# Performance work log

Measured on AMD Instinct MI355X. Metric: run time of the kernel, lower is better.

Reference implementation:

```python
import jax, jax.numpy as jnp
import numpy as np

BS, S, DM, H, DK, DV, PRED = 64, 128, 512, 8, 512, 512, 96
NF = S * DM  # Flatten_Head nf = patch_num * d_model
SCALE_INIT = (DM // H) ** (-0.5)  # head_dim from d_model//n_heads per _ScaledDotProductAttention


def setup_inputs() -> dict:
    key = jax.random.key(0)
    ks = jax.random.split(key, 24)
    g = lambda k, shp: (0.02 * jax.random.normal(k, shp)).astype(jnp.float32)
    inp = {
        "x": jax.random.normal(ks[0], (BS, S, DM), dtype=jnp.float32),
        "prev": jax.random.normal(ks[1], (BS, H, S, S), dtype=jnp.float32),
        # multi-head attention projections (d_k = d_v = d_model per TMBlock)
        "Wq": g(ks[2], (DM, H * DK)), "bq": jnp.zeros((H * DK,), jnp.float32),
        "Wk": g(ks[3], (DM, H * DK)), "bk": jnp.zeros((H * DK,), jnp.float32),
        "Wv": g(ks[4], (DM, H * DV)), "bv": jnp.zeros((H * DV,), jnp.float32),
        "Wo": g(ks[5], (H * DV, DM)), "bo": jnp.zeros((DM,), jnp.float32),
        "scale": jnp.float32(SCALE_INIT),
        # InterPatchMixing: Linear(PatchNum, PatchNum) x2
        "Wi1": g(ks[6], (S, S)), "bi1": jnp.zeros((S,), jnp.float32),
        "Wi2": g(ks[7], (S, S)), "bi2": jnp.zeros((S,), jnp.float32),
        # IntraPatchMixing: Linear(PatchEmbedDim, PatchEmbedDim) x2
        "Wt1": g(ks[8], (DM, DM)), "bt1": jnp.zeros((DM,), jnp.float32),
        "Wt2": g(ks[9], (DM, DM)), "bt2": jnp.zeros((DM,), jnp.float32),
        # Flatten_Head (non-individual): Linear(nf, pred_len)
        "Wh": g(ks[10], (NF, PRED)), "bh": jnp.zeros((PRED,), jnp.float32),
    }
    return inp


def reference(x, prev, Wq, bq, Wk, bk, Wv, bv, Wo, bo, scale,
              Wi1, bi1, Wi2, bi2, Wt1, bt1, Wt2, bt2, Wh, bh):
    bs = x.shape[0]
    # projections -> [bs, H, S, d]
    q = (x @ Wq + bq).reshape(bs, S, H, DK).transpose(0, 2, 1, 3)
    k = (x @ Wk + bk).reshape(bs, S, H, DK).transpose(0, 2, 1, 3)
    v = (x @ Wv + bv).reshape(bs, S, H, DV).transpose(0, 2, 1, 3)
    # manual scaled dot-product attention with residual attention bias (Realformer)
    scores = jnp.einsum('bhqd,bhkd->bhqk', q, k) * scale + prev
    attn = jax.nn.softmax(scores, axis=-1)  # dropout is identity at eval
    o = jnp.einsum('bhqk,bhkd->bhqd', attn, v)
    o = o.transpose(0, 2, 1, 3).reshape(bs, S, H * DV)
    o = o @ Wo + bo  # [bs, S, DM]
    # InterPatchMixing over the patch axis (last dim must be PatchNum)
    t = o.transpose(0, 2, 1)  # [bs, DM, S]
    t = jax.nn.relu(t @ Wi1 + bi1) @ Wi2 + bi2
    y = t.transpose(0, 2, 1)  # [bs, S, DM]
    # IntraPatchMixing over embed dim
    z = jax.nn.relu(y @ Wt1 + bt1) @ Wt2 + bt2
    # Flatten_Head: flatten last two dims -> Linear(nf, pred_len)
    out = z.reshape(bs, NF) @ Wh + bh  # [bs, PRED]
    return out
```

## Files before the change

### kernel.cpp

```cpp
#include <hip/hip_runtime.h>
#include <cstdint>
#include <cstddef>

typedef __bf16 bf16_t;
typedef __bf16 bf16x8 __attribute__((ext_vector_type(8)));
typedef __bf16 bf16x4 __attribute__((ext_vector_type(4)));
typedef float  f32x4  __attribute__((ext_vector_type(4)));

#define MFMA(a, b, c) __builtin_amdgcn_mfma_f32_16x16x32_bf16((a), (b), (c), 0, 0, 0)


__global__ __launch_bounds__(256) void k_convert_dual(const float* __restrict__ in,
                                                      bf16_t* __restrict__ xb,
                                                      bf16_t* __restrict__ xT) {
  __shared__ bf16_t tile[32][34];
  int tx = threadIdx.x & 31, ty = threadIdx.x >> 5;
  int c0 = blockIdx.x * 32, r0 = blockIdx.y * 32;
#pragma unroll
  for (int j = 0; j < 4; ++j) {
    int r = r0 + ty + j * 8;
    bf16_t bv = (bf16_t)in[(size_t)r * 512 + c0 + tx];
    xb[(size_t)r * 512 + c0 + tx] = bv;
    tile[ty + j * 8][tx] = bv;
  }
  __syncthreads();
  int b = (r0 + tx) >> 7, s = (r0 + tx) & 127;
#pragma unroll
  for (int j = 0; j < 4; ++j) {
    int i = c0 + ty + j * 8;
    xT[(size_t)b * 65536 + (size_t)i * 128 + s] = tile[tx][ty + j * 8];
  }
}

__global__ __launch_bounds__(256) void k_transpose_convert(const float* __restrict__ in,
                                                           bf16_t* __restrict__ out,
                                                           int R, int C) {
  __shared__ float tile[32][33];
  int tx = threadIdx.x & 31, ty = threadIdx.x >> 5;
  int c0 = blockIdx.x * 32, r0 = blockIdx.y * 32;
#pragma unroll
  for (int j = 0; j < 4; ++j)
    tile[ty + j * 8][tx] = in[(size_t)(r0 + ty + j * 8) * C + c0 + tx];
  __syncthreads();
#pragma unroll
  for (int j = 0; j < 4; ++j)
    out[(size_t)(c0 + ty + j * 8) * R + r0 + tx] = (bf16_t)tile[tx][ty + j * 8];
}

__global__ __launch_bounds__(256) void k_transpose_b16(const bf16_t* __restrict__ in,
                                                       bf16_t* __restrict__ out,
                                                       int R, int C) {
  __shared__ bf16_t tile[32][34];
  size_t base = (size_t)blockIdx.z * R * C;
  int tx = threadIdx.x & 31, ty = threadIdx.x >> 5;
  int c0 = blockIdx.x * 32, r0 = blockIdx.y * 32;
#pragma unroll
  for (int j = 0; j < 4; ++j)
    tile[ty + j * 8][tx] = in[base + (size_t)(r0 + ty + j * 8) * C + c0 + tx];
  __syncthreads();
#pragma unroll
  for (int j = 0; j < 4; ++j)
    out[base + (size_t)(c0 + ty + j * 8) * R + r0 + tx] = tile[tx][ty + j * 8];
}

template <int BMODE>
__global__ __launch_bounds__(256) void k_wprod(const float* __restrict__ Ap,
                                               const float* __restrict__ Bp,
                                               bf16_t* __restrict__ out,
                                               int ldA, int ldB) {
  __shared__ __align__(16) bf16_t As[128 * 68];
  __shared__ __align__(16) bf16_t Bs[128 * 68];
  const int tid = threadIdx.x, lane = tid & 63, wave = tid >> 6;
  const int wr = (wave >> 1) * 64, wc = (wave & 1) * 64;
  const int lr = lane & 15, lk = (lane >> 4) * 8, frow = (lane >> 4) * 4;
  const int m0 = blockIdx.x * 128, n0 = blockIdx.y * 128, h = blockIdx.z;
  const int sr = tid >> 3, sc = (tid & 7) * 8;
  f32x4 acc[4][4] = {};

  for (int kt = 0; kt < 512; kt += 64) {
#pragma unroll
    for (int rr = 0; rr < 4; ++rr) {
      int r = sr + 32 * rr;
      const float* ap = Ap + (size_t)(m0 + r) * ldA + h * 512 + kt + sc;
      bf16x8 av;
#pragma unroll
      for (int e = 0; e < 8; ++e) av[e] = (bf16_t)ap[e];
      *(bf16x8*)(As + r * 68 + sc) = av;
    }
    if (BMODE == 0) {
#pragma unroll
      for (int rr = 0; rr < 4; ++rr) {
        int r = sr + 32 * rr;
        const float* bp = Bp + (size_t)(n0 + r) * ldB + h * 512 + kt + sc;
        bf16x8 bv;
#pragma unroll
        for (int e = 0; e < 8; ++e) bv[e] = (bf16_t)bp[e];
        *(bf16x8*)(Bs + r * 68 + sc) = bv;
      }
    } else {
#pragma unroll
      for (int rr = 0; rr < 8; ++rr) {
        int kr = (tid >> 5) + 8 * rr;
        int nc = (tid & 31) * 4;
        const float* bp = Bp + (size_t)(h * 512 + kt + kr) * ldB + n0 + nc;
        float4 v = *(const float4*)bp;
        Bs[(nc + 0) * 68 + kr] = (bf16_t)v.x;
        Bs[(nc + 1) * 68 + kr] = (bf16_t)v.y;
        Bs[(nc + 2) * 68 + kr] = (bf16_t)v.z;
        Bs[(nc + 3) * 68 + kr] = (bf16_t)v.w;
      }
    }
    __syncthreads();
#pragma unroll
    for (int kk = 0; kk < 2; ++kk) {
      bf16x8 af[4], bfr[4];
#pragma unroll
      for (int i = 0; i < 4; ++i)
        af[i] = *(const bf16x8*)(As + (wr + i * 16 + lr) * 68 + kk * 32 + lk);
#pragma unroll
      for (int j = 0; j < 4; ++j)
        bfr[j] = *(const bf16x8*)(Bs + (wc + j * 16 + lr) * 68 + kk * 32 + lk);
#pragma unroll
      for (int i = 0; i < 4; ++i)
#pragma unroll
        for (int j = 0; j < 4; ++j)
          acc[i][j] = MFMA(af[i], bfr[j], acc[i][j]);
    }
    __syncthreads();
  }
#pragma unroll
  for (int i = 0; i < 4; ++i)
#pragma unroll
    for (int j = 0; j < 4; ++j)
#pragma unroll
      for (int q = 0; q < 4; ++q) {
        int gm = m0 + wr + i * 16 + frow + q;
        int gn = n0 + wc + j * 16 + lr;
        if (BMODE == 0)
          out[(size_t)(h * 512 + gn) * 512 + gm] = (bf16_t)acc[i][j][q];
        else
          out[(size_t)gn * 4096 + h * 512 + gm] = (bf16_t)acc[i][j][q];
      }
}

__global__ __launch_bounds__(256) void k_sbias(const float* __restrict__ Wq,
                                               const float* __restrict__ bk,
                                               const float* __restrict__ Wk,
                                               const float* __restrict__ bq,
                                               float* __restrict__ W1,
                                               float* __restrict__ W2,
                                               float* __restrict__ c) {
  const int lane = threadIdx.x & 63, wave = threadIdx.x >> 6;
  const int i = blockIdx.x * 4 + wave;
  for (int h = 0; h < 8; ++h) {
    float s1 = 0.f, s2 = 0.f;
    for (int d = lane; d < 512; d += 64) {
      s1 += Wq[(size_t)i * 4096 + h * 512 + d] * bk[h * 512 + d];
      s2 += Wk[(size_t)i * 4096 + h * 512 + d] * bq[h * 512 + d];
    }
#pragma unroll
    for (int o = 32; o > 0; o >>= 1) { s1 += __shfl_down(s1, o); s2 += __shfl_down(s2, o); }
    if (lane == 0) { W1[h * 512 + i] = s1; W2[h * 512 + i] = s2; }
  }
  if (blockIdx.x == 0 && wave == 0) {
    for (int h = 0; h < 8; ++h) {
      float cc = 0.f;
      for (int d = lane; d < 512; d += 64) cc += bq[h * 512 + d] * bk[h * 512 + d];
#pragma unroll
      for (int o = 32; o > 0; o >>= 1) cc += __shfl_down(cc, o);
      if (lane == 0) c[h] = cc;
    }
  }
}

__global__ __launch_bounds__(256) void k_tbias(const bf16_t* __restrict__ xb,
                                               const float* __restrict__ W1,
                                               const float* __restrict__ W2,
                                               const float* __restrict__ cb,
                                               float* __restrict__ TallT) {
  __shared__ float Ws[16][512];
  __shared__ float scr[128][32];
  const int tid = threadIdx.x;
  for (int i = tid; i < 4096; i += 256) {
    Ws[i >> 9][i & 511] = W1[i];
    Ws[8 + (i >> 9)][i & 511] = W2[i];
  }
  __syncthreads();
  const int rl = tid & 127, part = tid >> 7;
  const int row = blockIdx.x * 128 + rl;
  const bf16_t* xr = xb + (size_t)row * 512 + part * 256;
  float acc[16] = {};
  for (int i = 0; i < 256; i += 8) {
    bf16x8 xv = *(const bf16x8*)(xr + i);
#pragma unroll
    for (int e = 0; e < 8; ++e) {
      float f = (float)xv[e];
#pragma unroll
      for (int cI = 0; cI < 16; ++cI) acc[cI] += f * Ws[cI][part * 256 + i + e];
    }
  }
#pragma unroll
  for (int cI = 0; cI < 16; ++cI) scr[rl][part * 16 + cI] = acc[cI];
  __syncthreads();
  if (tid < 128) {
    int r = blockIdx.x * 128 + tid;
#pragma unroll
    for (int cI = 0; cI < 16; ++cI) {
      float v = scr[tid][cI] + scr[tid][16 + cI];
      if (cI < 8) v += cb[cI];
      TallT[cI * 8192 + r] = v;
    }
  }
}

__global__ __launch_bounds__(256) void k_cvec1(const float* __restrict__ bv,
                                               const float* __restrict__ Wo,
                                               float* __restrict__ cpart) {
  int cch = blockIdx.x, d = threadIdx.x * 2;
  float ax = 0.f, ay = 0.f;
  for (int n = cch * 128; n < cch * 128 + 128; ++n) {
    float b = bv[n];
    float2 w = *(const float2*)(Wo + (size_t)n * 512 + d);
    ax += b * w.x; ay += b * w.y;
  }
  cpart[(size_t)cch * 512 + d] = ax;
  cpart[(size_t)cch * 512 + d + 1] = ay;
}
__global__ __launch_bounds__(256) void k_cvec2(const float* __restrict__ cpart,
                                               const float* __restrict__ bo,
                                               float* __restrict__ cvec) {
  int d = blockIdx.x * 256 + threadIdx.x;
  float s = bo[d];
  for (int cch = 0; cch < 32; ++cch) s += cpart[(size_t)cch * 512 + d];
  cvec[d] = s;
}

__global__ __launch_bounds__(64, 2) void k_attn7(const bf16_t* __restrict__ xb,
                                                 const bf16_t* __restrict__ xT,
                                                 bf16_t* __restrict__ TU,
                                                 const float* __restrict__ prev,
                                                 const float* __restrict__ scale_p,
                                                 const float* __restrict__ TallT,
                                                 int hg) {
  __shared__ __align__(16) bf16_t Pl[16 * 136];
  __shared__ __align__(16) bf16_t Bw[16 * 72];

  const int lane = threadIdx.x;
  const int lr = lane & 15, lk = (lane >> 4) * 8, frow = (lane >> 4) * 4;
  const int bid = blockIdx.x;
  const int bx = (bid & 7) * 256 + (bid >> 3);
  const int b = bx >> 5, hp = (bx >> 3) & 3, rg = bx & 7;
  const int h = hg * 4 + hp;
  const int r0 = rg * 16;
  const bf16_t* xB = xb + (size_t)b * 65536;
  const bf16_t* xTB = xT + (size_t)b * 65536;
  bf16_t* tB = TU + ((size_t)hp * 8192 + b * 128 + r0) * 512;

  bf16_t tf_store[16 * 8];
  bf16x8* tf = (bf16x8*)tf_store;
  const bf16_t* aP = tB + (size_t)lr * 512 + lk;
#pragma unroll
  for (int kx = 0; kx < 16; ++kx) tf[kx] = *(const bf16x8*)(aP + kx * 32);

  const float* t1p = TallT + h * 8192 + b * 128 + r0;
  const float* t2p = TallT + (8 + h) * 8192 + b * 128;
  float pv[4][8];
#pragma unroll
  for (int e = 0; e < 4; ++e) {
    const float* prow = prev + (((size_t)(b * 8 + h)) * 128 + r0 + frow + e) * 128;
#pragma unroll
    for (int j = 0; j < 8; ++j) pv[e][j] = prow[j * 16 + lr];
  }
  float t1r[4];
#pragma unroll
  for (int e = 0; e < 4; ++e) t1r[e] = t1p[frow + e];
  float t2r[8];
#pragma unroll
  for (int j = 0; j < 8; ++j) t2r[j] = t2p[j * 16 + lr];

  f32x4 sacc[8] = {};
  const bf16_t* bP = xB + (size_t)lr * 512 + lk;
  __builtin_amdgcn_s_setprio(1);
#pragma unroll
  for (int kx = 0; kx < 16; ++kx) {
    bf16x8 bfr[8];
#pragma unroll
    for (int j = 0; j < 8; ++j)
      bfr[j] = *(const bf16x8*)(bP + (size_t)j * 8192 + kx * 32);
#pragma unroll
    for (int j = 0; j < 8; ++j) sacc[j] = MFMA(tf[kx], bfr[j], sacc[j]);
  }
  __builtin_amdgcn_s_setprio(0);

  const float scl = scale_p[0];
#pragma unroll
  for (int e = 0; e < 4; ++e) {
    const int rl = frow + e;
    float mx = -3.4e38f;
#pragma unroll
    for (int j = 0; j < 8; ++j) {
      float v = scl * (sacc[j][e] + t1r[e] + t2r[j]) + pv[e][j];
      sacc[j][e] = v;
      mx = fmaxf(mx, v);
    }
    mx = fmaxf(mx, __shfl_xor(mx, 1));
    mx = fmaxf(mx, __shfl_xor(mx, 2));
    mx = fmaxf(mx, __shfl_xor(mx, 4));
    mx = fmaxf(mx, __shfl_xor(mx, 8));
    float sum = 0.f;
#pragma unroll
    for (int j = 0; j < 8; ++j) {
      float p = __expf(sacc[j][e] - mx);
      sacc[j][e] = p;
      sum += p;
    }
    sum += __shfl_xor(sum, 1);
    sum += __shfl_xor(sum, 2);
    sum += __shfl_xor(sum, 4);
    sum += __shfl_xor(sum, 8);
    float inv = 1.f / sum;
#pragma unroll
    for (int j = 0; j < 8; ++j)
      Pl[rl * 136 + j * 16 + lr] = (bf16_t)(sacc[j][e] * inv);
  }

#pragma unroll
  for (int dc = 0; dc < 8; ++dc) {
    f32x4 oacc[4] = {};
    __builtin_amdgcn_s_setprio(1);
#pragma unroll
    for (int kk = 0; kk < 4; ++kk) {
      bf16x8 pa = *(const bf16x8*)(Pl + lr * 136 + kk * 32 + lk);
      bf16x8 xf[4];
#pragma unroll
      for (int j = 0; j < 4; ++j)
        xf[j] = *(const bf16x8*)(xTB + (size_t)(dc * 64 + j * 16 + lr) * 128 + kk * 32 + lk);
#pragma unroll
      for (int j = 0; j < 4; ++j) oacc[j] = MFMA(pa, xf[j], oacc[j]);
    }
    __builtin_amdgcn_s_setprio(0);
#pragma unroll
    for (int j = 0; j < 4; ++j)
#pragma unroll
      for (int e = 0; e < 4; ++e)
        Bw[(frow + e) * 72 + j * 16 + lr] = (bf16_t)oacc[j][e];
#pragma unroll
    for (int r2 = 0; r2 < 2; ++r2) {
      int row = lane >> 2, chunk = (lane & 3) + r2 * 4;
      *(bf16x8*)(tB + (size_t)row * 512 + dc * 64 + chunk * 8) =
          *(const bf16x8*)(Bw + row * 72 + chunk * 8);
    }
  }
}

template <int OUTMODE, int RELU>
__global__ __launch_bounds__(256) void k_gemm(const bf16_t* __restrict__ A,
                                              const bf16_t* __restrict__ Bt,
                                              const float* __restrict__ bias,
                                              bf16_t* __restrict__ C,
                                              int M, int N, int K) {
  __shared__ __align__(16) bf16_t As[128 * 68];
  __shared__ __align__(16) bf16_t Bs[128 * 68];
  const int tid = threadIdx.x, lane = tid & 63, wave = tid >> 6;
  const int wr = (wave >> 1) * 64, wc = (wave & 1) * 64;
  const int m0 = blockIdx.x * 128, n0 = blockIdx.y * 128;
  const int lr = lane & 15, lk = (lane >> 4) * 8, frow = (lane >> 4) * 4;
  const int sr = tid >> 3, sc = (tid & 7) * 8;
  f32x4 acc[4][4] = {};

  for (int kt = 0; kt < K; kt += 64) {
#pragma unroll
    for (int i = 0; i < 4; ++i) {
      int r = i * 32 + sr;
      *(bf16x8*)(As + r * 68 + sc) = *(const bf16x8*)(A + (size_t)(m0 + r) * K + kt + sc);
      *(bf16x8*)(Bs + r * 68 + sc) = *(const bf16x8*)(Bt + (size_t)(n0 + r) * K + kt + sc);
    }
    __syncthreads();
#pragma unroll
    for (int kk = 0; kk < 2; ++kk) {
      bf16x8 af[4], bfr[4];
#pragma unroll
      for (int i = 0; i < 4; ++i)
        af[i] = *(const bf16x8*)(As + (wr + i * 16 + lr) * 68 + kk * 32 + lk);
#pragma unroll
      for (int j = 0; j < 4; ++j)
        bfr[j] = *(const bf16x8*)(Bs + (wc + j * 16 + lr) * 68 + kk * 32 + lk);
#pragma unroll
      for (int i = 0; i < 4; ++i)
#pragma unroll
        for (int j = 0; j < 4; ++j)
          acc[i][j] = MFMA(af[i], bfr[j], acc[i][j]);
    }
    __syncthreads();
  }
#pragma unroll
  for (int j = 0; j < 4; ++j) {
    int gn = n0 + wc + j * 16 + lr;
    float bv = bias ? bias[gn] : 0.0f;
#pragma unroll
    for (int i = 0; i < 4; ++i) {
#pragma unroll
      for (int q = 0; q < 4; ++q) {
        int gm = m0 + wr + i * 16 + frow + q;
        float v = acc[i][j][q] + bv;
        if (RELU) v = v > 0.0f ? v : 0.0f;
        if (OUTMODE == 0)
          C[(size_t)gm * N + gn] = (bf16_t)v;
        else
          C[((size_t)(gn >> 9) * 8192 + gm) * 512 + (gn & 511)] = (bf16_t)v;
      }
    }
  }
}

template <int MODE>
__global__ __launch_bounds__(256) void k_gemm2(const bf16_t* __restrict__ U,
                                               const bf16_t* __restrict__ bt2,
                                               float* __restrict__ o1acc,
                                               const float* __restrict__ cvec,
                                               bf16_t* __restrict__ o1b, int g) {
  __shared__ __align__(16) bf16_t As[128 * 68];
  __shared__ __align__(16) bf16_t Bs[128 * 68];
  const int tid = threadIdx.x, lane = tid & 63, wave = tid >> 6;
  const int wr = (wave >> 1) * 64, wc = (wave & 1) * 64;
  const int m0 = blockIdx.x * 128, n0 = blockIdx.y * 128;
  const int lr = lane & 15, lk = (lane >> 4) * 8, frow = (lane >> 4) * 4;
  const int sr = tid >> 3, sc = (tid & 7) * 8;
  f32x4 acc[4][4] = {};

  for (int kt = 0; kt < 2048; kt += 64) {
    const int slab = kt >> 9, off = kt & 511;
#pragma unroll
    for (int i = 0; i < 4; ++i) {
      int r = i * 32 + sr;
      *(bf16x8*)(As + r * 68 + sc) =
          *(const bf16x8*)(U + ((size_t)slab * 8192 + m0 + r) * 512 + off + sc);
      *(bf16x8*)(Bs + r * 68 + sc) =
          *(const bf16x8*)(bt2 + (size_t)(n0 + r) * 4096 + g * 2048 + kt + sc);
    }
    __syncthreads();
#pragma unroll
    for (int kk = 0; kk < 2; ++kk) {
      bf16x8 af[4], bfr[4];
#pragma unroll
      for (int i = 0; i < 4; ++i)
        af[i] = *(const bf16x8*)(As + (wr + i * 16 + lr) * 68 + kk * 32 + lk);
#pragma unroll
      for (int j = 0; j < 4; ++j)
        bfr[j] = *(const bf16x8*)(Bs + (wc + j * 16 + lr) * 68 + kk * 32 + lk);
#pragma unroll
      for (int i = 0; i < 4; ++i)
#pragma unroll
        for (int j = 0; j < 4; ++j)
          acc[i][j] = MFMA(af[i], bfr[j], acc[i][j]);
    }
    __syncthreads();
  }
#pragma unroll
  for (int j = 0; j < 4; ++j) {
    int gn = n0 + wc + j * 16 + lr;
#pragma unroll
    for (int i = 0; i < 4; ++i) {
#pragma unroll
      for (int q = 0; q < 4; ++q) {
        int gm = m0 + wr + i * 16 + frow + q;
        size_t idx = (size_t)gm * 512 + gn;
        if (MODE == 0)
          o1acc[idx] = acc[i][j][q];
        else
          o1b[idx] = (bf16_t)(acc[i][j][q] + o1acc[idx] + cvec[gn]);
      }
    }
  }
}

__global__ __launch_bounds__(256) void k_head_partial(const bf16_t* __restrict__ Z,
                                                      const bf16_t* __restrict__ WhT,
                                                      float* __restrict__ part) {
  __shared__ __align__(16) bf16_t As[64 * 68];
  __shared__ __align__(16) bf16_t Bs[96 * 68];
  const int tid = threadIdx.x, lane = tid & 63, wave = tid >> 6;
  const int wr = (wave >> 1) * 32, wc = (wave & 1) * 48;
  const int lr = lane & 15, lk = (lane >> 4) * 8, frow = (lane >> 4) * 4;
  const int k0 = blockIdx.x * 512;
  const int sr = tid >> 3, sc = (tid & 7) * 8;
  f32x4 acc[2][3] = {};
  for (int kt = 0; kt < 512; kt += 64) {
#pragma unroll
    for (int i = 0; i < 2; ++i) {
      int r = i * 32 + sr;
      *(bf16x8*)(As + r * 68 + sc) = *(const bf16x8*)(Z + (size_t)r * 65536 + k0 + kt + sc);
    }
#pragma unroll
    for (int i = 0; i < 3; ++i) {
      int r = i * 32 + sr;
      *(bf16x8*)(Bs + r * 68 + sc) = *(const bf16x8*)(WhT + (size_t)r * 65536 + k0 + kt + sc);
    }
    __syncthreads();
#pragma unroll
    for (int kk = 0; kk < 2; ++kk) {
      bf16x8 af[2], bfr[3];
#pragma unroll
      for (int i = 0; i < 2; ++i)
        af[i] = *(const bf16x8*)(As + (wr + i * 16 + lr) * 68 + kk * 32 + lk);
#pragma unroll
      for (int j = 0; j < 3; ++j)
        bfr[j] = *(const bf16x8*)(Bs + (wc + j * 16 + lr) * 68 + kk * 32 + lk);
#pragma unroll
      for (int i = 0; i < 2; ++i)
#pragma unroll
        for (int j = 0; j < 3; ++j)
          acc[i][j] = MFMA(af[i], bfr[j], acc[i][j]);
    }
    __syncthreads();
  }
#pragma unroll
  for (int i = 0; i < 2; ++i)
#pragma unroll
    for (int j = 0; j < 3; ++j)
#pragma unroll
      for (int q = 0; q < 4; ++q) {
        int m = wr + i * 16 + frow + q;
        int n = wc + j * 16 + lr;
        part[(size_t)blockIdx.x * 6144 + m * 96 + n] = acc[i][j][q];
      }
}

__global__ __launch_bounds__(256) void k_head_reduce(const float* __restrict__ part,
                                                     const float* __restrict__ bias,
                                                     float* __restrict__ out) {
  int idx = blockIdx.x * 256 + threadIdx.x;
  if (idx >= 6144) return;
  float s = bias[idx % 96];
  for (int kb = 0; kb < 128; ++kb) s += part[(size_t)kb * 6144 + idx];
  out[idx] = s;
}

__global__ void k_sentinel(float* out, int n, float val) {
  int i = blockIdx.x * 256 + threadIdx.x;
  if (i < n) out[i] = val;
}

extern "C" void kernel_launch(void* const* d_in, const int* in_sizes, int n_in,
                              void* d_out, int out_size, void* d_ws, size_t ws_size,
                              hipStream_t stream) {
  const float* x    = (const float*)d_in[0];
  const float* prev = (const float*)d_in[1];
  const float* Wq = (const float*)d_in[2];   const float* bq = (const float*)d_in[3];
  const float* Wk = (const float*)d_in[4];   const float* bk = (const float*)d_in[5];
  const float* Wv = (const float*)d_in[6];   const float* bv = (const float*)d_in[7];
  const float* Wo = (const float*)d_in[8];   const float* bo = (const float*)d_in[9];
  const float* scale = (const float*)d_in[10];
  const float* Wi1 = (const float*)d_in[11]; const float* bi1 = (const float*)d_in[12];
  const float* Wi2 = (const float*)d_in[13]; const float* bi2 = (const float*)d_in[14];
  const float* Wt1 = (const float*)d_in[15]; const float* bt1w = (const float*)d_in[16];
  const float* Wt2 = (const float*)d_in[17]; const float* bt2w = (const float*)d_in[18];
  const float* Wh = (const float*)d_in[19];  const float* bh = (const float*)d_in[20];
  float* out = (float*)d_out;

  char* p = (char*)d_ws;
  auto carve = [&](size_t bytes) {
    char* r = p;
    p += (bytes + 255) & ~(size_t)255;
    return r;
  };
  bf16_t* xb    = (bf16_t*)carve((size_t)8192 * 512 * 2);
  bf16_t* xTo1b = (bf16_t*)carve((size_t)8192 * 512 * 2);
  float*  o1acc = (float*)carve((size_t)8192 * 512 * 4);
  bf16_t* bt1   = (bf16_t*)carve((size_t)4096 * 512 * 2);
  bf16_t* bt2   = (bf16_t*)carve((size_t)512 * 4096 * 2);
  float*  W1    = (float*)carve(8 * 512 * 4);
  float*  W2    = (float*)carve(8 * 512 * 4);
  float*  cb    = (float*)carve(8 * 4);
  float*  cvec  = (float*)carve(512 * 4);
  char*   arena = carve((size_t)8192 * 2048 * 2);
  bf16_t* TU    = (bf16_t*)arena;
  float*  cpart = (float*)arena;
  bf16_t* xT    = xTo1b;
  bf16_t* o1b   = xTo1b;
  float*  TallT = (float*)bt1;
  char* q2 = arena;
  auto carve2 = [&](size_t bytes) {
    char* r = q2;
    q2 += (bytes + 255) & ~(size_t)255;
    return r;
  };
  bf16_t* whT  = (bf16_t*)carve2((size_t)96 * 65536 * 2);
  bf16_t* wt1T = (bf16_t*)carve2((size_t)512 * 512 * 2);
  bf16_t* wt2T = (bf16_t*)carve2((size_t)512 * 512 * 2);
  bf16_t* wi1T = (bf16_t*)carve2((size_t)128 * 128 * 2);
  bf16_t* wi2T = (bf16_t*)carve2((size_t)128 * 128 * 2);
  float*  hp   = (float*)carve2((size_t)128 * 64 * 96 * 4);
  bf16_t* bufB = (bf16_t*)carve2((size_t)8192 * 512 * 2);

  if ((size_t)(p - (char*)d_ws) > ws_size) {
    k_sentinel<<<24, 256, 0, stream>>>(out, 6144, (float)ws_size);
    return;
  }

  dim3 blk(256);
  k_cvec1<<<32, blk, 0, stream>>>(bv, Wo, cpart);
  k_cvec2<<<2, blk, 0, stream>>>(cpart, bo, cvec);
  k_convert_dual<<<dim3(16, 256), blk, 0, stream>>>(x, xb, xT);
  k_wprod<0><<<dim3(4, 4, 8), blk, 0, stream>>>(Wq, Wk, bt1, 4096, 4096);
  k_wprod<1><<<dim3(4, 4, 8), blk, 0, stream>>>(Wv, Wo, bt2, 4096, 512);
  k_sbias<<<128, blk, 0, stream>>>(Wq, bk, Wk, bq, W1, W2, cb);

  k_gemm<2, 0><<<dim3(64, 16), blk, 0, stream>>>(xb, bt1, nullptr, TU, 8192, 2048, 512);
  k_tbias<<<64, blk, 0, stream>>>(xb, W1, W2, cb, TallT);
  k_attn7<<<2048, dim3(64), 0, stream>>>(xb, xT, TU, prev, scale, TallT, 0);
  k_gemm2<0><<<dim3(64, 4), blk, 0, stream>>>(TU, bt2, o1acc, cvec, o1b, 0);
  k_gemm<2, 0><<<dim3(64, 16), blk, 0, stream>>>(xb, bt1 + (size_t)2048 * 512, nullptr, TU,
                                                 8192, 2048, 512);
  k_attn7<<<2048, dim3(64), 0, stream>>>(xb, xT, TU, prev, scale, TallT, 1);
  k_gemm2<1><<<dim3(64, 4), blk, 0, stream>>>(TU, bt2, o1acc, cvec, o1b, 1);

  k_transpose_convert<<<dim3(4, 4), blk, 0, stream>>>(Wi1, wi1T, 128, 128);
  k_transpose_convert<<<dim3(4, 4), blk, 0, stream>>>(Wi2, wi2T, 128, 128);
  k_transpose_convert<<<dim3(16, 16), blk, 0, stream>>>(Wt1, wt1T, 512, 512);
  k_transpose_convert<<<dim3(16, 16), blk, 0, stream>>>(Wt2, wt2T, 512, 512);
  k_transpose_convert<<<dim3(3, 2048), blk, 0, stream>>>(Wh, whT, 65536, 96);

  k_transpose_b16<<<dim3(16, 4, 64), blk, 0, stream>>>(o1b, bufB, 128, 512);
  k_gemm<0, 1><<<dim3(256, 1), blk, 0, stream>>>(bufB, wi1T, bi1, o1b, 32768, 128, 128);
  k_gemm<0, 0><<<dim3(256, 1), blk, 0, stream>>>(o1b, wi2T, bi2, bufB, 32768, 128, 128);
  k_transpose_b16<<<dim3(4, 16, 64), blk, 0, stream>>>(bufB, o1b, 512, 128);

  k_gemm<0, 1><<<dim3(64, 4), blk, 0, stream>>>(o1b, wt1T, bt1w, bufB, 8192, 512, 512);
  k_gemm<0, 0><<<dim3(64, 4), blk, 0, stream>>>(bufB, wt2T, bt2w, o1b, 8192, 512, 512);

  k_head_partial<<<128, blk, 0, stream>>>(o1b, whT, hp);
  k_head_reduce<<<24, blk, 0, stream>>>(hp, bh, out);
}
```

Before: 492.3 us.

## Group eight attention waves per block with barriers to share batch data in cache

The single-wave attention kernel becomes a 512-thread block in which eight waves cover four heads and two 16-row groups of the same batch. Each wave gets its own LDS slices. Periodic s_barrier calls keep the waves in lockstep so they read the shared xb/xT rows at about the same time, which should help L1/L2 reuse. The cost is barrier stalls and coarser scheduling: 256 large blocks instead of 2048 small ones.

```diff
diff --git a/kernel.cpp b/kernel.cpp
--- a/kernel.cpp
+++ b/kernel.cpp
@@ -235,23 +235,25 @@
   cvec[d] = s;
 }
 
-__global__ __launch_bounds__(64, 2) void k_attn7(const bf16_t* __restrict__ xb,
-                                                 const bf16_t* __restrict__ xT,
-                                                 bf16_t* __restrict__ TU,
-                                                 const float* __restrict__ prev,
-                                                 const float* __restrict__ scale_p,
-                                                 const float* __restrict__ TallT,
-                                                 int hg) {
-  __shared__ __align__(16) bf16_t Pl[16 * 136];
-  __shared__ __align__(16) bf16_t Bw[16 * 72];
-
-  const int lane = threadIdx.x;
+__global__ __launch_bounds__(512, 2) void k_attn8(const bf16_t* __restrict__ xb,
+                                                  const bf16_t* __restrict__ xT,
+                                                  bf16_t* __restrict__ TU,
+                                                  const float* __restrict__ prev,
+                                                  const float* __restrict__ scale_p,
+                                                  const float* __restrict__ TallT,
+                                                  int hg) {
+  __shared__ __align__(16) bf16_t Pl[8][16 * 136];
+  __shared__ __align__(16) bf16_t Bw[8][16 * 72];
+
+  const int tid = threadIdx.x;
+  const int lane = tid & 63, wave = tid >> 6;
   const int lr = lane & 15, lk = (lane >> 4) * 8, frow = (lane >> 4) * 4;
   const int bid = blockIdx.x;
-  const int bx = (bid & 7) * 256 + (bid >> 3);
-  const int b = bx >> 5, hp = (bx >> 3) & 3, rg = bx & 7;
+  const int bx = (bid & 7) * 32 + (bid >> 3);
+  const int b = bx >> 2, rghi = bx & 3;
+  const int hp = wave & 3, rglo = wave >> 2;
   const int h = hg * 4 + hp;
-  const int r0 = rg * 16;
+  const int r0 = rghi * 32 + rglo * 16;
   const bf16_t* xB = xb + (size_t)b * 65536;
   const bf16_t* xTB = xT + (size_t)b * 65536;
   bf16_t* tB = TU + ((size_t)hp * 8192 + b * 128 + r0) * 512;
@@ -278,21 +280,29 @@
 #pragma unroll
   for (int j = 0; j < 8; ++j) t2r[j] = t2p[j * 16 + lr];
 
+  __builtin_amdgcn_s_barrier();
+
   f32x4 sacc[8] = {};
   const bf16_t* bP = xB + (size_t)lr * 512 + lk;
-  __builtin_amdgcn_s_setprio(1);
-#pragma unroll
-  for (int kx = 0; kx < 16; ++kx) {
-    bf16x8 bfr[8];
-#pragma unroll
-    for (int j = 0; j < 8; ++j)
-      bfr[j] = *(const bf16x8*)(bP + (size_t)j * 8192 + kx * 32);
-#pragma unroll
-    for (int j = 0; j < 8; ++j) sacc[j] = MFMA(tf[kx], bfr[j], sacc[j]);
-  }
-  __builtin_amdgcn_s_setprio(0);
+#pragma unroll
+  for (int kc = 0; kc < 4; ++kc) {
+    __builtin_amdgcn_s_setprio(1);
+#pragma unroll
+    for (int ki = 0; ki < 4; ++ki) {
+      const int kx = kc * 4 + ki;
+      bf16x8 bfr[8];
+#pragma unroll
+      for (int j = 0; j < 8; ++j)
+        bfr[j] = *(const bf16x8*)(bP + (size_t)j * 8192 + kx * 32);
+#pragma unroll
+      for (int j = 0; j < 8; ++j) sacc[j] = MFMA(tf[kx], bfr[j], sacc[j]);
+    }
+    __builtin_amdgcn_s_setprio(0);
+    __builtin_amdgcn_s_barrier();
+  }
 
   const float scl = scale_p[0];
+  bf16_t* Plw = Pl[wave];
 #pragma unroll
   for (int e = 0; e < 4; ++e) {
     const int rl = frow + e;
@@ -321,16 +331,18 @@
     float inv = 1.f / sum;
 #pragma unroll
     for (int j = 0; j < 8; ++j)
-      Pl[rl * 136 + j * 16 + lr] = (bf16_t)(sacc[j][e] * inv);
-  }
-
+      Plw[rl * 136 + j * 16 + lr] = (bf16_t)(sacc[j][e] * inv);
+  }
+  __builtin_amdgcn_s_barrier();
+
+  bf16_t* Bww = Bw[wave];
 #pragma unroll
   for (int dc = 0; dc < 8; ++dc) {
     f32x4 oacc[4] = {};
     __builtin_amdgcn_s_setprio(1);
 #pragma unroll
     for (int kk = 0; kk < 4; ++kk) {
-      bf16x8 pa = *(const bf16x8*)(Pl + lr * 136 + kk * 32 + lk);
+      bf16x8 pa = *(const bf16x8*)(Plw + lr * 136 + kk * 32 + lk);
       bf16x8 xf[4];
 #pragma unroll
       for (int j = 0; j < 4; ++j)
@@ -343,13 +355,14 @@
     for (int j = 0; j < 4; ++j)
 #pragma unroll
       for (int e = 0; e < 4; ++e)
-        Bw[(frow + e) * 72 + j * 16 + lr] = (bf16_t)oacc[j][e];
+        Bww[(frow + e) * 72 + j * 16 + lr] = (bf16_t)oacc[j][e];
 #pragma unroll
     for (int r2 = 0; r2 < 2; ++r2) {
       int row = lane >> 2, chunk = (lane & 3) + r2 * 4;
       *(bf16x8*)(tB + (size_t)row * 512 + dc * 64 + chunk * 8) =
-          *(const bf16x8*)(Bw + row * 72 + chunk * 8);
-    }
+          *(const bf16x8*)(Bww + row * 72 + chunk * 8);
+    }
+    if (dc == 1 || dc == 3 || dc == 5) __builtin_amdgcn_s_barrier();
   }
 }
 
@@ -608,11 +621,11 @@
 
   k_gemm<2, 0><<<dim3(64, 16), blk, 0, stream>>>(xb, bt1, nullptr, TU, 8192, 2048, 512);
   k_tbias<<<64, blk, 0, stream>>>(xb, W1, W2, cb, TallT);
-  k_attn7<<<2048, dim3(64), 0, stream>>>(xb, xT, TU, prev, scale, TallT, 0);
+  k_attn8<<<256, dim3(512), 0, stream>>>(xb, xT, TU, prev, scale, TallT, 0);
   k_gemm2<0><<<dim3(64, 4), blk, 0, stream>>>(TU, bt2, o1acc, cvec, o1b, 0);
   k_gemm<2, 0><<<dim3(64, 16), blk, 0, stream>>>(xb, bt1 + (size_t)2048 * 512, nullptr, TU,
                                                  8192, 2048, 512);
-  k_attn7<<<2048, dim3(64), 0, stream>>>(xb, xT, TU, prev, scale, TallT, 1);
+  k_attn8<<<256, dim3(512), 0, stream>>>(xb, xT, TU, prev, scale, TallT, 1);
   k_gemm2<1><<<dim3(64, 4), blk, 0, stream>>>(TU, bt2, o1acc, cvec, o1b, 1);
 
   k_transpose_convert<<<dim3(4, 4), blk, 0, stream>>>(Wi1, wi1T, 128, 128);
```

Result: no change. 497.8 us (+1.1%).
